# Optimization experiments

Hardware: AMD Instinct MI355X
Metric: run time of the kernel (lower is better)

Reference implementation:

```python
import jax, jax.numpy as jnp
import numpy as np

FIELD_DIMS = [26000] * 39
EMBED_DIM = 64
MLP_DIMS = [400, 400, 400]
BATCH = 16384
OFFSETS = jnp.asarray(np.concatenate(([0], np.cumsum(FIELD_DIMS)[:-1])), dtype=jnp.int32)
BN_INV = 1.0 / np.sqrt(1.0 + 1e-5)  # eval-mode BatchNorm1d: running_mean=0, running_var=1


def setup_inputs() -> dict:
    key = jax.random.key(0)
    ks = jax.random.split(key, 16)
    B, F, E = BATCH, len(FIELD_DIMS), EMBED_DIM
    V = sum(FIELD_DIMS)
    s = lambda k, shp, sc=0.05: (jax.random.normal(k, shp, jnp.float32) * sc)
    inp = {
        "x": jax.random.randint(ks[0], (B, F), 0, FIELD_DIMS[0], dtype=jnp.int32),
        "emb_table": s(ks[1], (V, E)),
        "lin_table": s(ks[2], (V, 1)),
        "lin_bias": jnp.zeros((1,), jnp.float32),
        "sparse_var": s(ks[3], (F, E), 0.1),
        "Wt": s(ks[4], (F, E, E)),  # per-field Linear weights, (out,in) layout
        "bt": jnp.zeros((F, E), jnp.float32),
    }
    dims = [F * E] + MLP_DIMS
    for i in range(3):
        inp[f"W{i+1}"] = s(ks[5 + i], (dims[i], dims[i + 1]))
        inp[f"b{i+1}"] = jnp.zeros((dims[i + 1],), jnp.float32)
        inp[f"g{i+1}"] = jnp.ones((dims[i + 1],), jnp.float32)
        inp[f"be{i+1}"] = jnp.zeros((dims[i + 1],), jnp.float32)
    inp["Wout"] = s(ks[9], (MLP_DIMS[-1], 1))
    inp["bout"] = jnp.zeros((1,), jnp.float32)
    return inp


def reference(x, emb_table, lin_table, lin_bias, sparse_var, Wt, bt,
              W1, b1, g1, be1, W2, b2, g2, be2, W3, b3, g3, be3, Wout, bout):
    B = x.shape[0]
    idx = x + OFFSETS[None, :]                       # (B, F) global vocab ids
    # sparse gate (detached in torch), eval-mode hard threshold mask
    sv = jax.nn.sigmoid(jax.lax.stop_gradient(sparse_var) * 15.0)
    sv = jnp.where(sv > 0.001, sv, 0.0)              # (F, E)
    embed_x = emb_table[idx] * sv                    # (B, F, E) gather + gate
    # per-field small Linear, batched as one einsum (torch: y = e @ W.T + b)
    trans = jnp.einsum('bfi,foi->bfo', embed_x, Wt) + bt  # (B, F, E)
    # FM second-order term
    sum_f = trans.sum(axis=1)                        # (B, E)
    fm = 0.5 * jnp.sum(sum_f * sum_f - (trans * trans).sum(axis=1),
                       axis=-1, keepdims=True)       # (B, 1)
    # first-order linear term
    lin = lin_table[idx].sum(axis=1) + lin_bias      # (B, 1)
    # MLP on flattened gated embeddings (Linear -> BN(eval) -> ReLU)
    h = embed_x.reshape(B, -1)
    for W, b, g, be in ((W1, b1, g1, be1), (W2, b2, g2, be2), (W3, b3, g3, be3)):
        h = jax.nn.relu((h @ W + b) * (BN_INV * g) + be)
    mlp = h @ Wout + bout                            # (B, 1)
    return jax.nn.sigmoid(jnp.squeeze(lin + fm + mlp, axis=1))  # (B,)
```

## Files before the change

kernel.cpp:

```cpp
#include <hip/hip_runtime.h>

#define BT 16384
#define NF 39
#define FD 26000

typedef unsigned short u16;
typedef unsigned int u32;
typedef short bf16x8 __attribute__((ext_vector_type(8)));
typedef float f32x4 __attribute__((ext_vector_type(4)));

__device__ __forceinline__ float bf2f(u16 h) {
  union { u32 u; float f; } v; v.u = ((u32)h) << 16; return v.f;
}
__device__ __forceinline__ u16 f2bf(float f) {
  union { float f; u32 u; } v; v.f = f;
  u32 r = v.u + 0x7fffu + ((v.u >> 16) & 1u);
  return (u16)(r >> 16);
}
__device__ __forceinline__ void gld16(const u16* g, u16* l) {
  __builtin_amdgcn_global_load_lds(
      (const __attribute__((address_space(1))) void*)g,
      (__attribute__((address_space(3))) void*)l, 16, 0, 0);
}

__global__ __launch_bounds__(256) void k_prep(
    const float* __restrict__ W1, u16* __restrict__ W1T,
    const float* __restrict__ W2, u16* __restrict__ W2T,
    const float* __restrict__ W3, u16* __restrict__ W3T,
    const float* __restrict__ Wt, u16* __restrict__ Wtb)
{
  int z = blockIdx.z;
  if (z == 3) {
    int idx = (blockIdx.y * 14 + blockIdx.x) * 256 + threadIdx.x;
    if (idx < NF * 4096) Wtb[idx] = f2bf(Wt[idx]);
    return;
  }
  const float* in = (z == 0) ? W1 : (z == 1) ? W2 : W3;
  u16* outp = (z == 0) ? W1T : (z == 1) ? W2T : W3T;
  int K = (z == 0) ? 2496 : 400;
  int Kpad = (z == 0) ? 2496 : 448;
  int r0 = blockIdx.y * 32, c0 = blockIdx.x * 32;
  if (r0 >= Kpad) return;
  __shared__ u16 t[32][33];
  int tx = threadIdx.x & 31, ty = threadIdx.x >> 5;
  for (int i = ty; i < 32; i += 8) {
    int r = r0 + i, c = c0 + tx;
    t[i][tx] = (r < K && c < 400) ? f2bf(in[(long)r * 400 + c]) : (u16)0;
  }
  __syncthreads();
  int r = r0 + tx;
  if (r < Kpad)
    for (int i = ty; i < 32; i += 8)
      outp[(long)(c0 + i) * Kpad + r] = t[tx][i];
}

__global__ __launch_bounds__(256) void k_embed(
    const int* __restrict__ x, const float* __restrict__ emb,
    const float* __restrict__ lin_table, const float* __restrict__ lin_bias,
    const float* __restrict__ sparse_var, const u16* __restrict__ Wtb,
    const float* __restrict__ bt, u16* __restrict__ h0, float* __restrict__ base)
{
  __shared__ u16                s_x[32 * NF];
  __shared__ float              s_sv[NF * 64];
  __shared__ float              s_bt[NF * 64];
  __shared__ __align__(16) u16  s_emb[2][32 * 72];
  __shared__ __align__(16) u16  s_wt[2][64 * 64];
  __shared__ float              s_fm[64];
  __shared__ float              s_lin[32];

  const int tid = threadIdx.x;
  const int b0 = blockIdx.x * 32;

  for (int i = tid; i < 32 * NF; i += 256) s_x[i] = (u16)x[b0 * NF + i];
  for (int i = tid; i < NF * 64; i += 256) {
    float v = sparse_var[i];
    float s = 1.0f / (1.0f + __expf(-15.0f * v));
    s_sv[i] = (s > 0.001f) ? s : 0.0f;
    s_bt[i] = bt[i];
  }
  __syncthreads();

  const int wave = tid >> 6, lane = tid & 63;
  const int quad = lane >> 4, c16 = lane & 15;
  const int mt = wave & 1, nh = wave >> 1;
  const int g_row = tid >> 3, g_c8 = (tid & 7) * 8;
  const int wrow = lane >> 3;
  const int wchk = (lane & 7) ^ wrow;

  float q[4] = {0.f, 0.f, 0.f, 0.f};
  float accS[2][4] = {{0.f,0.f,0.f,0.f},{0.f,0.f,0.f,0.f}};

  #pragma unroll
  for (int i = 0; i < 2; ++i) {
    int ii = wave * 2 + i;
    gld16(Wtb + (ii * 8 + wrow) * 64 + wchk * 8, &s_wt[0][ii * 512]);
  }
  {
    long gi = (long)((int)s_x[g_row * NF + 0]);
    float4 e0 = *(const float4*)&emb[gi * 64 + g_c8];
    float4 e1 = *(const float4*)&emb[gi * 64 + g_c8 + 4];
    union { uint4 v; u16 h[8]; } p;
    p.h[0] = f2bf(e0.x * s_sv[g_c8 + 0]);
    p.h[1] = f2bf(e0.y * s_sv[g_c8 + 1]);
    p.h[2] = f2bf(e0.z * s_sv[g_c8 + 2]);
    p.h[3] = f2bf(e0.w * s_sv[g_c8 + 3]);
    p.h[4] = f2bf(e1.x * s_sv[g_c8 + 4]);
    p.h[5] = f2bf(e1.y * s_sv[g_c8 + 5]);
    p.h[6] = f2bf(e1.z * s_sv[g_c8 + 6]);
    p.h[7] = f2bf(e1.w * s_sv[g_c8 + 7]);
    *(uint4*)&s_emb[0][g_row * 72 + g_c8] = p.v;
    *(uint4*)&h0[(long)(b0 + g_row) * 2496 + g_c8] = p.v;
  }
  __syncthreads();

  for (int f = 0; f < NF; ++f) {
    const int cur = f & 1, nxt = cur ^ 1;
    float4 e0, e1;
    const bool more = (f + 1) < NF;
    if (more) {
      #pragma unroll
      for (int i = 0; i < 2; ++i) {
        int ii = wave * 2 + i;
        gld16(Wtb + (f + 1) * 4096 + (ii * 8 + wrow) * 64 + wchk * 8,
              &s_wt[nxt][ii * 512]);
      }
      long gi = (long)((int)s_x[g_row * NF + f + 1] + (f + 1) * FD);
      e0 = *(const float4*)&emb[gi * 64 + g_c8];
      e1 = *(const float4*)&emb[gi * 64 + g_c8 + 4];
    }

    bf16x8 a0 = *(const bf16x8*)&s_emb[cur][(mt * 16 + c16) * 72 + quad * 8];
    bf16x8 a1 = *(const bf16x8*)&s_emb[cur][(mt * 16 + c16) * 72 + 32 + quad * 8];
    #pragma unroll
    for (int j = 0; j < 2; ++j) {
      int row = (nh * 2 + j) * 16 + c16;
      int pc0 = quad ^ (row & 7);
      int pc1 = (quad + 4) ^ (row & 7);
      bf16x8 bb0 = *(const bf16x8*)&s_wt[cur][row * 64 + pc0 * 8];
      bf16x8 bb1 = *(const bf16x8*)&s_wt[cur][row * 64 + pc1 * 8];
      f32x4 acc = {0.f, 0.f, 0.f, 0.f};
      acc = __builtin_amdgcn_mfma_f32_16x16x32_bf16(a0, bb0, acc, 0, 0, 0);
      acc = __builtin_amdgcn_mfma_f32_16x16x32_bf16(a1, bb1, acc, 0, 0, 0);
      float btv = s_bt[f * 64 + row];
      #pragma unroll
      for (int r = 0; r < 4; ++r) {
        float t = acc[r] + btv;
        accS[j][r] += t;
        q[r] += t * t;
      }
    }

    if (more) {
      union { uint4 v; u16 h[8]; } p;
      const float* sv = &s_sv[(f + 1) * 64 + g_c8];
      p.h[0] = f2bf(e0.x * sv[0]);
      p.h[1] = f2bf(e0.y * sv[1]);
      p.h[2] = f2bf(e0.z * sv[2]);
      p.h[3] = f2bf(e0.w * sv[3]);
      p.h[4] = f2bf(e1.x * sv[4]);
      p.h[5] = f2bf(e1.y * sv[5]);
      p.h[6] = f2bf(e1.z * sv[6]);
      p.h[7] = f2bf(e1.w * sv[7]);
      *(uint4*)&s_emb[nxt][g_row * 72 + g_c8] = p.v;
      *(uint4*)&h0[(long)(b0 + g_row) * 2496 + (f + 1) * 64 + g_c8] = p.v;
    }
    __syncthreads();
  }

  #pragma unroll
  for (int r = 0; r < 4; ++r) {
    float v = accS[0][r] * accS[0][r] + accS[1][r] * accS[1][r] - q[r];
    v += __shfl_xor(v, 1, 64);
    v += __shfl_xor(v, 2, 64);
    v += __shfl_xor(v, 4, 64);
    v += __shfl_xor(v, 8, 64);
    if (c16 == 0) s_fm[nh * 32 + mt * 16 + quad * 4 + r] = v;
  }
  {
    int row = tid >> 3, fi = tid & 7;
    float lv = 0.f;
    for (int f = fi; f < NF; f += 8)
      lv += lin_table[(int)s_x[row * NF + f] + f * FD];
    lv += __shfl_xor(lv, 1, 64);
    lv += __shfl_xor(lv, 2, 64);
    lv += __shfl_xor(lv, 4, 64);
    if (fi == 0) s_lin[row] = lv;
  }
  __syncthreads();
  if (tid < 32)
    base[b0 + tid] = s_lin[tid] + lin_bias[0]
                   + 0.5f * (s_fm[tid] + s_fm[32 + tid]);
}

__global__ __launch_bounds__(256) void k_gemm(
    const u16* __restrict__ A, int lda, const u16* __restrict__ Bt, int ldb,
    int kit, const float* __restrict__ bias, const float* __restrict__ g,
    const float* __restrict__ be, u16* __restrict__ C, int ldc)
{
  __shared__ __align__(16) u16 sA[128 * 64];
  __shared__ __align__(16) u16 sB[80 * 64];

  const int tid = threadIdx.x;
  int bid = blockIdx.x;
  int xcd = bid & 7;
  int j = bid >> 3;
  const int m0 = (xcd * 16 + j / 5) * 128;
  const int n0 = (j % 5) * 80;

  const int wave = tid >> 6, lane = tid & 63;
  const int quad = lane >> 4, c16 = lane & 15;

  const int srow = lane >> 3;
  const int sclog = (lane & 7) ^ (srow & 7);
  const u16* gA = A + (long)m0 * lda + sclog * 8;
  const u16* gB = Bt + (long)n0 * ldb + sclog * 8;

  f32x4 acc[2][5];
  #pragma unroll
  for (int mtt = 0; mtt < 2; ++mtt)
    #pragma unroll
    for (int nt = 0; nt < 5; ++nt) acc[mtt][nt] = {0.f, 0.f, 0.f, 0.f};

  for (int kk = 0; kk < kit; ++kk) {
    const int k0 = kk * 64;
    #pragma unroll
    for (int it = 0; it < 4; ++it) {
      int s = wave * 4 + it;
      gld16(gA + (long)(s * 8 + srow) * lda + k0, &sA[s * 512]);
    }
    gld16(gB + (long)(wave * 8 + srow) * ldb + k0, &sB[wave * 512]);
    gld16(gB + (long)((wave + 4) * 8 + srow) * ldb + k0, &sB[(wave + 4) * 512]);
    if (wave < 2)
      gld16(gB + (long)((wave + 8) * 8 + srow) * ldb + k0, &sB[(wave + 8) * 512]);
    __syncthreads();

    #pragma unroll
    for (int ks = 0; ks < 2; ++ks) {
      const int co = ((ks * 4 + quad) ^ (c16 & 7)) * 8;
      bf16x8 a0 = *(const bf16x8*)&sA[(wave * 32 + c16) * 64 + co];
      bf16x8 a1 = *(const bf16x8*)&sA[(wave * 32 + 16 + c16) * 64 + co];
      #pragma unroll
      for (int nt = 0; nt < 5; ++nt) {
        bf16x8 b = *(const bf16x8*)&sB[(nt * 16 + c16) * 64 + co];
        acc[0][nt] = __builtin_amdgcn_mfma_f32_16x16x32_bf16(a0, b, acc[0][nt], 0, 0, 0);
        acc[1][nt] = __builtin_amdgcn_mfma_f32_16x16x32_bf16(a1, b, acc[1][nt], 0, 0, 0);
      }
    }
    __syncthreads();
  }

  const float BN_INV = 0.9999950000374997f;
  #pragma unroll
  for (int nt = 0; nt < 5; ++nt) {
    int col = n0 + nt * 16 + c16;
    float bb = bias[col];
    float sc = BN_INV * g[col];
    float bv = be[col];
    #pragma unroll
    for (int mtt = 0; mtt < 2; ++mtt) {
      #pragma unroll
      for (int r = 0; r < 4; ++r) {
        int row = m0 + wave * 32 + mtt * 16 + quad * 4 + r;
        float y = (acc[mtt][nt][r] + bb) * sc + bv;
        y = fmaxf(y, 0.f);
        C[(long)row * ldc + col] = f2bf(y);
      }
    }
  }
  if (ldc > 400 && n0 == 320) {
    int npad = ldc - 400;
    for (int s = tid; s < 128 * npad; s += 256) {
      int rr = s / npad, cc = s % npad;
      C[(long)(m0 + rr) * ldc + 400 + cc] = 0;
    }
  }
}

__global__ __launch_bounds__(256) void k_final(
    const u16* __restrict__ h3, const float* __restrict__ Wout,
    const float* __restrict__ bout, const float* __restrict__ base,
    float* __restrict__ out)
{
  int wave = threadIdx.x >> 6, lane = threadIdx.x & 63;
  int b = blockIdx.x * 4 + wave;
  float s = 0.f;
  for (int jj = lane; jj < 400; jj += 64)
    s += bf2f(h3[(long)b * 448 + jj]) * Wout[jj];
  #pragma unroll
  for (int m = 32; m >= 1; m >>= 1) s += __shfl_xor(s, m, 64);
  if (lane == 0) {
    float z = s + base[b] + bout[0];
    out[b] = 1.0f / (1.0f + __expf(-z));
  }
}

extern "C" void kernel_launch(void* const* d_in, const int* in_sizes, int n_in,
                              void* d_out, int out_size, void* d_ws, size_t ws_size,
                              hipStream_t stream)
{
  const int*   x         = (const int*)d_in[0];
  const float* emb       = (const float*)d_in[1];
  const float* lin_table = (const float*)d_in[2];
  const float* lin_bias  = (const float*)d_in[3];
  const float* svar      = (const float*)d_in[4];
  const float* Wt        = (const float*)d_in[5];
  const float* bt        = (const float*)d_in[6];
  const float* W1  = (const float*)d_in[7];
  const float* b1  = (const float*)d_in[8];
  const float* g1  = (const float*)d_in[9];
  const float* be1 = (const float*)d_in[10];
  const float* W2  = (const float*)d_in[11];
  const float* b2  = (const float*)d_in[12];
  const float* g2  = (const float*)d_in[13];
  const float* be2 = (const float*)d_in[14];
  const float* W3  = (const float*)d_in[15];
  const float* b3  = (const float*)d_in[16];
  const float* g3  = (const float*)d_in[17];
  const float* be3 = (const float*)d_in[18];
  const float* Wo  = (const float*)d_in[19];
  const float* bo  = (const float*)d_in[20];

  char* ws = (char*)d_ws;
  size_t off = 0;
  u16* h0 = (u16*)(ws + off);     off += (size_t)BT * 2496 * 2;
  u16* h1 = (u16*)(ws + off);     off += (size_t)BT * 448 * 2;
  u16* h2 = (u16*)(ws + off);     off += (size_t)BT * 448 * 2;
  u16* h3 = (u16*)(ws + off);     off += (size_t)BT * 448 * 2;
  float* base = (float*)(ws + off); off += (size_t)BT * 4;
  u16* W1T = (u16*)(ws + off);    off += (size_t)448 * 2496 * 2;
  u16* W2T = (u16*)(ws + off);    off += (size_t)448 * 448 * 2;
  u16* W3T = (u16*)(ws + off);    off += (size_t)448 * 448 * 2;
  u16* Wtb = (u16*)(ws + off);    off += (size_t)NF * 4096 * 2;
  (void)ws_size; (void)in_sizes; (void)n_in; (void)out_size;

  k_prep<<<dim3(14, 78, 4), 256, 0, stream>>>(W1, W1T, W2, W2T, W3, W3T, Wt, Wtb);
  k_embed<<<512, 256, 0, stream>>>(x, emb, lin_table, lin_bias, svar, Wtb, bt,
                                   h0, base);
  k_gemm<<<640, 256, 0, stream>>>(h0, 2496, W1T, 2496, 39, b1, g1, be1, h1, 448);
  k_gemm<<<640, 256, 0, stream>>>(h1, 448, W2T, 448, 7, b2, g2, be2, h2, 448);
  k_gemm<<<640, 256, 0, stream>>>(h2, 448, W3T, 448, 7, b3, g3, be3, h3, 448);
  k_final<<<4096, 256, 0, stream>>>(h3, Wo, bo, base, (float*)d_out);
}
```

Before: 477.2 us.

## Fuse embedding gather, FM transform and first MLP layer into one kernel

The embedding/FM kernel now also computes the first MLP layer. For each field it streams the matching 64-wide K-slice of W1T into LDS with double buffering and accumulates a 64x448 output tile in registers, then applies bias, BN and ReLU and writes h1 directly. This removes the write and re-read of the large h0 activation buffer and one kernel launch. In exchange each block streams the whole W1T (256 blocks, 64 rows each, one block per CU by launch bounds), register pressure rises to 112 accumulators, and per-field Wt fragments are now read from global memory instead of LDS.

New measurement: 1.030 ms. +115.8%, slower.

```diff
diff --git a/kernel.cpp b/kernel.cpp
--- a/kernel.cpp
+++ b/kernel.cpp
@@ -54,142 +54,233 @@
       outp[(long)(c0 + i) * Kpad + r] = t[tx][i];
 }
 
-__global__ __launch_bounds__(256) void k_embed(
+__global__ __launch_bounds__(256, 1) void k_embed_mlp1(
     const int* __restrict__ x, const float* __restrict__ emb,
     const float* __restrict__ lin_table, const float* __restrict__ lin_bias,
     const float* __restrict__ sparse_var, const u16* __restrict__ Wtb,
-    const float* __restrict__ bt, u16* __restrict__ h0, float* __restrict__ base)
+    const float* __restrict__ bt, const u16* __restrict__ W1T,
+    const float* __restrict__ b1, const float* __restrict__ g1,
+    const float* __restrict__ be1, u16* __restrict__ h1,
+    float* __restrict__ base)
 {
-  __shared__ u16                s_x[32 * NF];
+  __shared__ u16                s_x[64 * NF];
   __shared__ float              s_sv[NF * 64];
-  __shared__ float              s_bt[NF * 64];
-  __shared__ __align__(16) u16  s_emb[2][32 * 72];
-  __shared__ __align__(16) u16  s_wt[2][64 * 64];
-  __shared__ float              s_fm[64];
-  __shared__ float              s_lin[32];
+  __shared__ __align__(16) u16  s_emb[2][64 * 72];
+  __shared__ __align__(16) u16  s_w1[2][448 * 64];
+  __shared__ float              s_fm[128];
+  __shared__ float              s_lin[64];
 
   const int tid = threadIdx.x;
-  const int b0 = blockIdx.x * 32;
-
-  for (int i = tid; i < 32 * NF; i += 256) s_x[i] = (u16)x[b0 * NF + i];
+  const int b0 = blockIdx.x * 64;
+
+  for (int i = tid; i < 64 * NF; i += 256) s_x[i] = (u16)x[b0 * NF + i];
   for (int i = tid; i < NF * 64; i += 256) {
     float v = sparse_var[i];
     float s = 1.0f / (1.0f + __expf(-15.0f * v));
     s_sv[i] = (s > 0.001f) ? s : 0.0f;
-    s_bt[i] = bt[i];
   }
   __syncthreads();
 
   const int wave = tid >> 6, lane = tid & 63;
   const int quad = lane >> 4, c16 = lane & 15;
-  const int mt = wave & 1, nh = wave >> 1;
-  const int g_row = tid >> 3, g_c8 = (tid & 7) * 8;
-  const int wrow = lane >> 3;
-  const int wchk = (lane & 7) ^ wrow;
-
-  float q[4] = {0.f, 0.f, 0.f, 0.f};
-  float accS[2][4] = {{0.f,0.f,0.f,0.f},{0.f,0.f,0.f,0.f}};
-
-  #pragma unroll
-  for (int i = 0; i < 2; ++i) {
-    int ii = wave * 2 + i;
-    gld16(Wtb + (ii * 8 + wrow) * 64 + wchk * 8, &s_wt[0][ii * 512]);
+  const int mh = wave >> 1, jh = wave & 1;
+  const int g_row = tid >> 2, g_c16 = (tid & 3) * 16;
+  const int srow = lane >> 3;
+  const u16* gW = W1T + ((lane & 7) ^ srow) * 8;
+
+  f32x4 acc[7][4];
+  #pragma unroll
+  for (int nt = 0; nt < 7; ++nt)
+    #pragma unroll
+    for (int m = 0; m < 4; ++m) acc[nt][m] = {0.f, 0.f, 0.f, 0.f};
+  float accS[2][2][4];
+  float q[2][4];
+  #pragma unroll
+  for (int ml = 0; ml < 2; ++ml)
+    #pragma unroll
+    for (int r = 0; r < 4; ++r) {
+      accS[ml][0][r] = 0.f; accS[ml][1][r] = 0.f; q[ml][r] = 0.f;
+    }
+
+  #pragma unroll
+  for (int it = 0; it < 14; ++it) {
+    int s = wave * 14 + it;
+    gld16(gW + (long)(s * 8 + srow) * 2496, &s_w1[0][s * 512]);
   }
   {
     long gi = (long)((int)s_x[g_row * NF + 0]);
-    float4 e0 = *(const float4*)&emb[gi * 64 + g_c8];
-    float4 e1 = *(const float4*)&emb[gi * 64 + g_c8 + 4];
-    union { uint4 v; u16 h[8]; } p;
-    p.h[0] = f2bf(e0.x * s_sv[g_c8 + 0]);
-    p.h[1] = f2bf(e0.y * s_sv[g_c8 + 1]);
-    p.h[2] = f2bf(e0.z * s_sv[g_c8 + 2]);
-    p.h[3] = f2bf(e0.w * s_sv[g_c8 + 3]);
-    p.h[4] = f2bf(e1.x * s_sv[g_c8 + 4]);
-    p.h[5] = f2bf(e1.y * s_sv[g_c8 + 5]);
-    p.h[6] = f2bf(e1.z * s_sv[g_c8 + 6]);
-    p.h[7] = f2bf(e1.w * s_sv[g_c8 + 7]);
-    *(uint4*)&s_emb[0][g_row * 72 + g_c8] = p.v;
-    *(uint4*)&h0[(long)(b0 + g_row) * 2496 + g_c8] = p.v;
+    const float* src = emb + gi * 64 + g_c16;
+    float4 e0 = *(const float4*)(src);
+    float4 e1 = *(const float4*)(src + 4);
+    float4 e2 = *(const float4*)(src + 8);
+    float4 e3 = *(const float4*)(src + 12);
+    const float* svp = &s_sv[g_c16];
+    float4 s0 = *(const float4*)(svp);
+    float4 s1 = *(const float4*)(svp + 4);
+    float4 s2 = *(const float4*)(svp + 8);
+    float4 s3 = *(const float4*)(svp + 12);
+    union { uint4 v; u16 h[8]; } p0, p1;
+    p0.h[0] = f2bf(e0.x * s0.x); p0.h[1] = f2bf(e0.y * s0.y);
+    p0.h[2] = f2bf(e0.z * s0.z); p0.h[3] = f2bf(e0.w * s0.w);
+    p0.h[4] = f2bf(e1.x * s1.x); p0.h[5] = f2bf(e1.y * s1.y);
+    p0.h[6] = f2bf(e1.z * s1.z); p0.h[7] = f2bf(e1.w * s1.w);
+    p1.h[0] = f2bf(e2.x * s2.x); p1.h[1] = f2bf(e2.y * s2.y);
+    p1.h[2] = f2bf(e2.z * s2.z); p1.h[3] = f2bf(e2.w * s2.w);
+    p1.h[4] = f2bf(e3.x * s3.x); p1.h[5] = f2bf(e3.y * s3.y);
+    p1.h[6] = f2bf(e3.z * s3.z); p1.h[7] = f2bf(e3.w * s3.w);
+    *(uint4*)&s_emb[0][g_row * 72 + g_c16] = p0.v;
+    *(uint4*)&s_emb[0][g_row * 72 + g_c16 + 8] = p1.v;
   }
   __syncthreads();
 
   for (int f = 0; f < NF; ++f) {
     const int cur = f & 1, nxt = cur ^ 1;
-    float4 e0, e1;
     const bool more = (f + 1) < NF;
+
     if (more) {
       #pragma unroll
-      for (int i = 0; i < 2; ++i) {
-        int ii = wave * 2 + i;
-        gld16(Wtb + (f + 1) * 4096 + (ii * 8 + wrow) * 64 + wchk * 8,
-              &s_wt[nxt][ii * 512]);
-      }
+      for (int it = 0; it < 14; ++it) {
+        int s = wave * 14 + it;
+        gld16(gW + (long)(s * 8 + srow) * 2496 + (f + 1) * 64,
+              &s_w1[nxt][s * 512]);
+      }
+    }
+
+    bf16x8 bwt[2][2];
+    float btv[2];
+    #pragma unroll
+    for (int j = 0; j < 2; ++j) {
+      int o = (jh * 2 + j) * 16 + c16;
+      bwt[j][0] = *(const bf16x8*)(Wtb + f * 4096 + o * 64 + quad * 8);
+      bwt[j][1] = *(const bf16x8*)(Wtb + f * 4096 + o * 64 + 32 + quad * 8);
+      btv[j] = bt[f * 64 + o];
+    }
+
+    float4 e0, e1, e2, e3;
+    if (more) {
       long gi = (long)((int)s_x[g_row * NF + f + 1] + (f + 1) * FD);
-      e0 = *(const float4*)&emb[gi * 64 + g_c8];
-      e1 = *(const float4*)&emb[gi * 64 + g_c8 + 4];
-    }
-
-    bf16x8 a0 = *(const bf16x8*)&s_emb[cur][(mt * 16 + c16) * 72 + quad * 8];
-    bf16x8 a1 = *(const bf16x8*)&s_emb[cur][(mt * 16 + c16) * 72 + 32 + quad * 8];
-    #pragma unroll
-    for (int j = 0; j < 2; ++j) {
-      int row = (nh * 2 + j) * 16 + c16;
-      int pc0 = quad ^ (row & 7);
-      int pc1 = (quad + 4) ^ (row & 7);
-      bf16x8 bb0 = *(const bf16x8*)&s_wt[cur][row * 64 + pc0 * 8];
-      bf16x8 bb1 = *(const bf16x8*)&s_wt[cur][row * 64 + pc1 * 8];
-      f32x4 acc = {0.f, 0.f, 0.f, 0.f};
-      acc = __builtin_amdgcn_mfma_f32_16x16x32_bf16(a0, bb0, acc, 0, 0, 0);
-      acc = __builtin_amdgcn_mfma_f32_16x16x32_bf16(a1, bb1, acc, 0, 0, 0);
-      float btv = s_bt[f * 64 + row];
-      #pragma unroll
-      for (int r = 0; r < 4; ++r) {
-        float t = acc[r] + btv;
-        accS[j][r] += t;
-        q[r] += t * t;
+      const float* src = emb + gi * 64 + g_c16;
+      e0 = *(const float4*)(src);
+      e1 = *(const float4*)(src + 4);
+      e2 = *(const float4*)(src + 8);
+      e3 = *(const float4*)(src + 12);
+    }
+
+    bf16x8 a[4][2];
+    #pragma unroll
+    for (int m = 0; m < 4; ++m) {
+      #pragma unroll
+      for (int ks = 0; ks < 2; ++ks)
+        a[m][ks] = *(const bf16x8*)
+            &s_emb[cur][(m * 16 + c16) * 72 + ks * 32 + quad * 8];
+    }
+
+    #pragma unroll
+    for (int nt = 0; nt < 7; ++nt) {
+      int n = wave * 112 + nt * 16 + c16;
+      #pragma unroll
+      for (int ks = 0; ks < 2; ++ks) {
+        bf16x8 b = *(const bf16x8*)
+            &s_w1[cur][n * 64 + (((ks * 4 + quad) ^ (c16 & 7)) * 8)];
+        #pragma unroll
+        for (int m = 0; m < 4; ++m)
+          acc[nt][m] = __builtin_amdgcn_mfma_f32_16x16x32_bf16(
+              a[m][ks], b, acc[nt][m], 0, 0, 0);
+      }
+    }
+
+    #pragma unroll
+    for (int mloc = 0; mloc < 2; ++mloc) {
+      int m = mh * 2 + mloc;
+      #pragma unroll
+      for (int j = 0; j < 2; ++j) {
+        f32x4 t = {0.f, 0.f, 0.f, 0.f};
+        t = __builtin_amdgcn_mfma_f32_16x16x32_bf16(a[m][0], bwt[j][0], t, 0, 0, 0);
+        t = __builtin_amdgcn_mfma_f32_16x16x32_bf16(a[m][1], bwt[j][1], t, 0, 0, 0);
+        #pragma unroll
+        for (int r = 0; r < 4; ++r) {
+          float tv = t[r] + btv[j];
+          accS[mloc][j][r] += tv;
+          q[mloc][r] += tv * tv;
+        }
       }
     }
 
     if (more) {
-      union { uint4 v; u16 h[8]; } p;
-      const float* sv = &s_sv[(f + 1) * 64 + g_c8];
-      p.h[0] = f2bf(e0.x * sv[0]);
-      p.h[1] = f2bf(e0.y * sv[1]);
-      p.h[2] = f2bf(e0.z * sv[2]);
-      p.h[3] = f2bf(e0.w * sv[3]);
-      p.h[4] = f2bf(e1.x * sv[4]);
-      p.h[5] = f2bf(e1.y * sv[5]);
-      p.h[6] = f2bf(e1.z * sv[6]);
-      p.h[7] = f2bf(e1.w * sv[7]);
-      *(uint4*)&s_emb[nxt][g_row * 72 + g_c8] = p.v;
-      *(uint4*)&h0[(long)(b0 + g_row) * 2496 + (f + 1) * 64 + g_c8] = p.v;
+      const float* svp = &s_sv[(f + 1) * 64 + g_c16];
+      float4 s0 = *(const float4*)(svp);
+      float4 s1 = *(const float4*)(svp + 4);
+      float4 s2 = *(const float4*)(svp + 8);
+      float4 s3 = *(const float4*)(svp + 12);
+      union { uint4 v; u16 h[8]; } p0, p1;
+      p0.h[0] = f2bf(e0.x * s0.x); p0.h[1] = f2bf(e0.y * s0.y);
+      p0.h[2] = f2bf(e0.z * s0.z); p0.h[3] = f2bf(e0.w * s0.w);
+      p0.h[4] = f2bf(e1.x * s1.x); p0.h[5] = f2bf(e1.y * s1.y);
+      p0.h[6] = f2bf(e1.z * s1.z); p0.h[7] = f2bf(e1.w * s1.w);
+      p1.h[0] = f2bf(e2.x * s2.x); p1.h[1] = f2bf(e2.y * s2.y);
+      p1.h[2] = f2bf(e2.z * s2.z); p1.h[3] = f2bf(e2.w * s2.w);
+      p1.h[4] = f2bf(e3.x * s3.x); p1.h[5] = f2bf(e3.y * s3.y);
+      p1.h[6] = f2bf(e3.z * s3.z); p1.h[7] = f2bf(e3.w * s3.w);
+      *(uint4*)&s_emb[nxt][g_row * 72 + g_c16] = p0.v;
+      *(uint4*)&s_emb[nxt][g_row * 72 + g_c16 + 8] = p1.v;
     }
     __syncthreads();
   }
 
-  #pragma unroll
-  for (int r = 0; r < 4; ++r) {
-    float v = accS[0][r] * accS[0][r] + accS[1][r] * accS[1][r] - q[r];
-    v += __shfl_xor(v, 1, 64);
-    v += __shfl_xor(v, 2, 64);
-    v += __shfl_xor(v, 4, 64);
-    v += __shfl_xor(v, 8, 64);
-    if (c16 == 0) s_fm[nh * 32 + mt * 16 + quad * 4 + r] = v;
+  const float BN_INV = 0.9999950000374997f;
+  #pragma unroll
+  for (int nt = 0; nt < 7; ++nt) {
+    int col = wave * 112 + nt * 16 + c16;
+    if (col < 400) {
+      float bb = b1[col];
+      float sc = BN_INV * g1[col];
+      float bv = be1[col];
+      #pragma unroll
+      for (int m = 0; m < 4; ++m) {
+        #pragma unroll
+        for (int r = 0; r < 4; ++r) {
+          int row = b0 + m * 16 + quad * 4 + r;
+          float y = (acc[nt][m][r] + bb) * sc + bv;
+          y = fmaxf(y, 0.f);
+          h1[(long)row * 448 + col] = f2bf(y);
+        }
+      }
+    } else {
+      #pragma unroll
+      for (int m = 0; m < 4; ++m)
+        #pragma unroll
+        for (int r = 0; r < 4; ++r)
+          h1[(long)(b0 + m * 16 + quad * 4 + r) * 448 + col] = 0;
+    }
+  }
+
+  #pragma unroll
+  for (int mloc = 0; mloc < 2; ++mloc) {
+    #pragma unroll
+    for (int r = 0; r < 4; ++r) {
+      float v = accS[mloc][0][r] * accS[mloc][0][r]
+              + accS[mloc][1][r] * accS[mloc][1][r] - q[mloc][r];
+      v += __shfl_xor(v, 1, 64);
+      v += __shfl_xor(v, 2, 64);
+      v += __shfl_xor(v, 4, 64);
+      v += __shfl_xor(v, 8, 64);
+      if (c16 == 0)
+        s_fm[jh * 64 + (mh * 2 + mloc) * 16 + quad * 4 + r] = v;
+    }
   }
   {
-    int row = tid >> 3, fi = tid & 7;
+    int row = tid >> 2, fi = tid & 3;
     float lv = 0.f;
-    for (int f = fi; f < NF; f += 8)
+    for (int f = fi; f < NF; f += 4)
       lv += lin_table[(int)s_x[row * NF + f] + f * FD];
     lv += __shfl_xor(lv, 1, 64);
     lv += __shfl_xor(lv, 2, 64);
-    lv += __shfl_xor(lv, 4, 64);
     if (fi == 0) s_lin[row] = lv;
   }
   __syncthreads();
-  if (tid < 32)
+  if (tid < 64)
     base[b0 + tid] = s_lin[tid] + lin_bias[0]
-                   + 0.5f * (s_fm[tid] + s_fm[32 + tid]);
+                   + 0.5f * (s_fm[tid] + s_fm[64 + tid]);
 }
 
 __global__ __launch_bounds__(256) void k_gemm(
@@ -322,7 +413,6 @@
 
   char* ws = (char*)d_ws;
   size_t off = 0;
-  u16* h0 = (u16*)(ws + off);     off += (size_t)BT * 2496 * 2;
   u16* h1 = (u16*)(ws + off);     off += (size_t)BT * 448 * 2;
   u16* h2 = (u16*)(ws + off);     off += (size_t)BT * 448 * 2;
   u16* h3 = (u16*)(ws + off);     off += (size_t)BT * 448 * 2;
@@ -334,9 +424,8 @@
   (void)ws_size; (void)in_sizes; (void)n_in; (void)out_size;
 
   k_prep<<<dim3(14, 78, 4), 256, 0, stream>>>(W1, W1T, W2, W2T, W3, W3T, Wt, Wtb);
-  k_embed<<<512, 256, 0, stream>>>(x, emb, lin_table, lin_bias, svar, Wtb, bt,
-                                   h0, base);
-  k_gemm<<<640, 256, 0, stream>>>(h0, 2496, W1T, 2496, 39, b1, g1, be1, h1, 448);
+  k_embed_mlp1<<<256, 256, 0, stream>>>(x, emb, lin_table, lin_bias, svar, Wtb,
+                                        bt, W1T, b1, g1, be1, h1, base);
   k_gemm<<<640, 256, 0, stream>>>(h1, 448, W2T, 448, 7, b2, g2, be2, h2, 448);
   k_gemm<<<640, 256, 0, stream>>>(h2, 448, W3T, 448, 7, b3, g3, be3, h3, 448);
   k_final<<<4096, 256, 0, stream>>>(h3, Wo, bo, base, (float*)d_out);
```

## Fuse embedding gather with first MLP GEMM to skip materializing h0

Applied to the files above, without the earlier changes.

The embedding kernel now multiplies each field's gated 32x64 embedding tile directly against the matching W1T slice. Both the per-field transform weights and the W1 fragments are read straight from global memory into registers, and results accumulate into 32x448 tiles held in registers. The BN and ReLU epilogue is applied before writing h1, so the separate first GEMM launch and the large bf16 h0 write and re-read are removed. In exchange each 32-row block streams all of W1T through L2 with a small M tile and no LDS staging. That means much more L2 traffic, higher register pressure and exposed load latency inside the per-field loop.

Measured after the change: 533.9 us. 1.12x slower.

```diff
diff --git a/kernel.cpp b/kernel.cpp
--- a/kernel.cpp
+++ b/kernel.cpp
@@ -54,18 +54,20 @@
       outp[(long)(c0 + i) * Kpad + r] = t[tx][i];
 }
 
-__global__ __launch_bounds__(256) void k_embed(
+__global__ __launch_bounds__(256) void k_embed_mlp1(
     const int* __restrict__ x, const float* __restrict__ emb,
     const float* __restrict__ lin_table, const float* __restrict__ lin_bias,
     const float* __restrict__ sparse_var, const u16* __restrict__ Wtb,
-    const float* __restrict__ bt, u16* __restrict__ h0, float* __restrict__ base)
+    const float* __restrict__ bt, const u16* __restrict__ W1T,
+    const float* __restrict__ b1, const float* __restrict__ g1,
+    const float* __restrict__ be1, u16* __restrict__ h1,
+    float* __restrict__ base)
 {
   __shared__ u16                s_x[32 * NF];
   __shared__ float              s_sv[NF * 64];
   __shared__ float              s_bt[NF * 64];
   __shared__ __align__(16) u16  s_emb[2][32 * 72];
-  __shared__ __align__(16) u16  s_wt[2][64 * 64];
-  __shared__ float              s_fm[64];
+  __shared__ float              s_fm[4][32];
   __shared__ float              s_lin[32];
 
   const int tid = threadIdx.x;
@@ -82,19 +84,23 @@
 
   const int wave = tid >> 6, lane = tid & 63;
   const int quad = lane >> 4, c16 = lane & 15;
-  const int mt = wave & 1, nh = wave >> 1;
   const int g_row = tid >> 3, g_c8 = (tid & 7) * 8;
-  const int wrow = lane >> 3;
-  const int wchk = (lane & 7) ^ wrow;
-
-  float q[4] = {0.f, 0.f, 0.f, 0.f};
-  float accS[2][4] = {{0.f,0.f,0.f,0.f},{0.f,0.f,0.f,0.f}};
-
-  #pragma unroll
-  for (int i = 0; i < 2; ++i) {
-    int ii = wave * 2 + i;
-    gld16(Wtb + (ii * 8 + wrow) * 64 + wchk * 8, &s_wt[0][ii * 512]);
-  }
+
+  const u16* w1p = W1T + (long)(wave * 112 + c16) * 2496 + quad * 8;
+  const u16* wtp = Wtb + (long)(wave * 16 + c16) * 64 + quad * 8;
+
+  f32x4 acc[7][2];
+  #pragma unroll
+  for (int nt = 0; nt < 7; ++nt) {
+    acc[nt][0] = {0.f, 0.f, 0.f, 0.f};
+    acc[nt][1] = {0.f, 0.f, 0.f, 0.f};
+  }
+  float accS[2][4], q[2][4];
+  #pragma unroll
+  for (int m = 0; m < 2; ++m)
+    #pragma unroll
+    for (int r = 0; r < 4; ++r) { accS[m][r] = 0.f; q[m][r] = 0.f; }
+
   {
     long gi = (long)((int)s_x[g_row * NF + 0]);
     float4 e0 = *(const float4*)&emb[gi * 64 + g_c8];
@@ -109,50 +115,61 @@
     p.h[6] = f2bf(e1.z * s_sv[g_c8 + 6]);
     p.h[7] = f2bf(e1.w * s_sv[g_c8 + 7]);
     *(uint4*)&s_emb[0][g_row * 72 + g_c8] = p.v;
-    *(uint4*)&h0[(long)(b0 + g_row) * 2496 + g_c8] = p.v;
   }
   __syncthreads();
 
   for (int f = 0; f < NF; ++f) {
     const int cur = f & 1, nxt = cur ^ 1;
+    const bool more = (f + 1) < NF;
+
+    bf16x8 bwt0 = *(const bf16x8*)(wtp + f * 4096);
+    bf16x8 bwt1 = *(const bf16x8*)(wtp + f * 4096 + 32);
+    float btv = s_bt[f * 64 + wave * 16 + c16];
+
     float4 e0, e1;
-    const bool more = (f + 1) < NF;
     if (more) {
-      #pragma unroll
-      for (int i = 0; i < 2; ++i) {
-        int ii = wave * 2 + i;
-        gld16(Wtb + (f + 1) * 4096 + (ii * 8 + wrow) * 64 + wchk * 8,
-              &s_wt[nxt][ii * 512]);
-      }
       long gi = (long)((int)s_x[g_row * NF + f + 1] + (f + 1) * FD);
       e0 = *(const float4*)&emb[gi * 64 + g_c8];
       e1 = *(const float4*)&emb[gi * 64 + g_c8 + 4];
     }
 
-    bf16x8 a0 = *(const bf16x8*)&s_emb[cur][(mt * 16 + c16) * 72 + quad * 8];
-    bf16x8 a1 = *(const bf16x8*)&s_emb[cur][(mt * 16 + c16) * 72 + 32 + quad * 8];
-    #pragma unroll
-    for (int j = 0; j < 2; ++j) {
-      int row = (nh * 2 + j) * 16 + c16;
-      int pc0 = quad ^ (row & 7);
-      int pc1 = (quad + 4) ^ (row & 7);
-      bf16x8 bb0 = *(const bf16x8*)&s_wt[cur][row * 64 + pc0 * 8];
-      bf16x8 bb1 = *(const bf16x8*)&s_wt[cur][row * 64 + pc1 * 8];
-      f32x4 acc = {0.f, 0.f, 0.f, 0.f};
-      acc = __builtin_amdgcn_mfma_f32_16x16x32_bf16(a0, bb0, acc, 0, 0, 0);
-      acc = __builtin_amdgcn_mfma_f32_16x16x32_bf16(a1, bb1, acc, 0, 0, 0);
-      float btv = s_bt[f * 64 + row];
+    bf16x8 a[2][2];
+    #pragma unroll
+    for (int m = 0; m < 2; ++m)
+      #pragma unroll
+      for (int ks = 0; ks < 2; ++ks)
+        a[m][ks] = *(const bf16x8*)
+            &s_emb[cur][(m * 16 + c16) * 72 + ks * 32 + quad * 8];
+
+    const u16* w1f = w1p + f * 64;
+    #pragma unroll
+    for (int nt = 0; nt < 7; ++nt) {
+      #pragma unroll
+      for (int ks = 0; ks < 2; ++ks) {
+        bf16x8 b = *(const bf16x8*)(w1f + (long)nt * 16 * 2496 + ks * 32);
+        acc[nt][0] = __builtin_amdgcn_mfma_f32_16x16x32_bf16(
+            a[0][ks], b, acc[nt][0], 0, 0, 0);
+        acc[nt][1] = __builtin_amdgcn_mfma_f32_16x16x32_bf16(
+            a[1][ks], b, acc[nt][1], 0, 0, 0);
+      }
+    }
+
+    #pragma unroll
+    for (int m = 0; m < 2; ++m) {
+      f32x4 t = {0.f, 0.f, 0.f, 0.f};
+      t = __builtin_amdgcn_mfma_f32_16x16x32_bf16(a[m][0], bwt0, t, 0, 0, 0);
+      t = __builtin_amdgcn_mfma_f32_16x16x32_bf16(a[m][1], bwt1, t, 0, 0, 0);
       #pragma unroll
       for (int r = 0; r < 4; ++r) {
-        float t = acc[r] + btv;
-        accS[j][r] += t;
-        q[r] += t * t;
+        float tv = t[r] + btv;
+        accS[m][r] += tv;
+        q[m][r] += tv * tv;
       }
     }
 
     if (more) {
+      const float* sv = &s_sv[(f + 1) * 64 + g_c8];
       union { uint4 v; u16 h[8]; } p;
-      const float* sv = &s_sv[(f + 1) * 64 + g_c8];
       p.h[0] = f2bf(e0.x * sv[0]);
       p.h[1] = f2bf(e0.y * sv[1]);
       p.h[2] = f2bf(e0.z * sv[2]);
@@ -162,19 +179,48 @@
       p.h[6] = f2bf(e1.z * sv[6]);
       p.h[7] = f2bf(e1.w * sv[7]);
       *(uint4*)&s_emb[nxt][g_row * 72 + g_c8] = p.v;
-      *(uint4*)&h0[(long)(b0 + g_row) * 2496 + (f + 1) * 64 + g_c8] = p.v;
     }
     __syncthreads();
   }
 
-  #pragma unroll
-  for (int r = 0; r < 4; ++r) {
-    float v = accS[0][r] * accS[0][r] + accS[1][r] * accS[1][r] - q[r];
-    v += __shfl_xor(v, 1, 64);
-    v += __shfl_xor(v, 2, 64);
-    v += __shfl_xor(v, 4, 64);
-    v += __shfl_xor(v, 8, 64);
-    if (c16 == 0) s_fm[nh * 32 + mt * 16 + quad * 4 + r] = v;
+  const float BN_INV = 0.9999950000374997f;
+  #pragma unroll
+  for (int nt = 0; nt < 7; ++nt) {
+    int col = wave * 112 + nt * 16 + c16;
+    if (col < 400) {
+      float bb = b1[col];
+      float sc = BN_INV * g1[col];
+      float bv = be1[col];
+      #pragma unroll
+      for (int m = 0; m < 2; ++m) {
+        #pragma unroll
+        for (int r = 0; r < 4; ++r) {
+          int row = b0 + m * 16 + quad * 4 + r;
+          float y = (acc[nt][m][r] + bb) * sc + bv;
+          y = fmaxf(y, 0.f);
+          h1[(long)row * 448 + col] = f2bf(y);
+        }
+      }
+    } else {
+      #pragma unroll
+      for (int m = 0; m < 2; ++m)
+        #pragma unroll
+        for (int r = 0; r < 4; ++r)
+          h1[(long)(b0 + m * 16 + quad * 4 + r) * 448 + col] = 0;
+    }
+  }
+
+  #pragma unroll
+  for (int m = 0; m < 2; ++m) {
+    #pragma unroll
+    for (int r = 0; r < 4; ++r) {
+      float v = accS[m][r] * accS[m][r] - q[m][r];
+      v += __shfl_xor(v, 1, 64);
+      v += __shfl_xor(v, 2, 64);
+      v += __shfl_xor(v, 4, 64);
+      v += __shfl_xor(v, 8, 64);
+      if (c16 == 0) s_fm[wave][m * 16 + quad * 4 + r] = v;
+    }
   }
   {
     int row = tid >> 3, fi = tid & 7;
@@ -189,7 +235,8 @@
   __syncthreads();
   if (tid < 32)
     base[b0 + tid] = s_lin[tid] + lin_bias[0]
-                   + 0.5f * (s_fm[tid] + s_fm[32 + tid]);
+                   + 0.5f * (s_fm[0][tid] + s_fm[1][tid]
+                           + s_fm[2][tid] + s_fm[3][tid]);
 }
 
 __global__ __launch_bounds__(256) void k_gemm(
@@ -322,7 +369,6 @@
 
   char* ws = (char*)d_ws;
   size_t off = 0;
-  u16* h0 = (u16*)(ws + off);     off += (size_t)BT * 2496 * 2;
   u16* h1 = (u16*)(ws + off);     off += (size_t)BT * 448 * 2;
   u16* h2 = (u16*)(ws + off);     off += (size_t)BT * 448 * 2;
   u16* h3 = (u16*)(ws + off);     off += (size_t)BT * 448 * 2;
@@ -334,9 +380,8 @@
   (void)ws_size; (void)in_sizes; (void)n_in; (void)out_size;
 
   k_prep<<<dim3(14, 78, 4), 256, 0, stream>>>(W1, W1T, W2, W2T, W3, W3T, Wt, Wtb);
-  k_embed<<<512, 256, 0, stream>>>(x, emb, lin_table, lin_bias, svar, Wtb, bt,
-                                   h0, base);
-  k_gemm<<<640, 256, 0, stream>>>(h0, 2496, W1T, 2496, 39, b1, g1, be1, h1, 448);
+  k_embed_mlp1<<<512, 256, 0, stream>>>(x, emb, lin_table, lin_bias, svar, Wtb,
+                                        bt, W1T, b1, g1, be1, h1, base);
   k_gemm<<<640, 256, 0, stream>>>(h1, 448, W2T, 448, 7, b2, g2, be2, h2, 448);
   k_gemm<<<640, 256, 0, stream>>>(h2, 448, W3T, 448, 7, b3, g3, be3, h3, 448);
   k_final<<<4096, 256, 0, stream>>>(h3, Wo, bo, base, (float*)d_out);
```

## Split embed kernel fields across waves with register-resident operands and no per-field barriers

Applied to the files above, without the earlier changes.

The embedding/FM kernel now handles 16 rows per block, and each wave takes a strided subset of fields instead of all waves cooperating on every field. Embedding rows are gathered straight into registers as MFMA A-operands, with a one-step register prefetch. Per-field weights are read from global memory, so the LDS double buffering and the per-field __syncthreads are gone. Partial FM sums are reduced across waves through shared memory at the end. The intent is to remove 39 block barriers and raise parallelism (twice as many blocks, launch bounds set for occupancy), at the cost of more global weight traffic per block.

Result: slower. 503.9 us (+5.6%).

```diff
diff --git a/kernel.cpp b/kernel.cpp
--- a/kernel.cpp
+++ b/kernel.cpp
@@ -54,24 +54,24 @@
       outp[(long)(c0 + i) * Kpad + r] = t[tx][i];
 }
 
-__global__ __launch_bounds__(256) void k_embed(
+__global__ __launch_bounds__(256, 4) void k_embed(
     const int* __restrict__ x, const float* __restrict__ emb,
     const float* __restrict__ lin_table, const float* __restrict__ lin_bias,
     const float* __restrict__ sparse_var, const u16* __restrict__ Wtb,
     const float* __restrict__ bt, u16* __restrict__ h0, float* __restrict__ base)
 {
-  __shared__ u16                s_x[32 * NF];
-  __shared__ float              s_sv[NF * 64];
-  __shared__ float              s_bt[NF * 64];
-  __shared__ __align__(16) u16  s_emb[2][32 * 72];
-  __shared__ __align__(16) u16  s_wt[2][64 * 64];
-  __shared__ float              s_fm[64];
-  __shared__ float              s_lin[32];
+  __shared__ u16   s_x[16 * NF];
+  __shared__ float s_sv[NF * 64];
+  __shared__ float s_bt[NF * 64];
+  __shared__ float s_acc[3][16][64];
+  __shared__ float s_q[3][4][64];
+  __shared__ float s_fm[16];
+  __shared__ float s_lin[16];
 
   const int tid = threadIdx.x;
-  const int b0 = blockIdx.x * 32;
-
-  for (int i = tid; i < 32 * NF; i += 256) s_x[i] = (u16)x[b0 * NF + i];
+  const int b0 = blockIdx.x * 16;
+
+  for (int i = tid; i < 16 * NF; i += 256) s_x[i] = (u16)x[b0 * NF + i];
   for (int i = tid; i < NF * 64; i += 256) {
     float v = sparse_var[i];
     float s = 1.0f / (1.0f + __expf(-15.0f * v));
@@ -82,114 +82,117 @@
 
   const int wave = tid >> 6, lane = tid & 63;
   const int quad = lane >> 4, c16 = lane & 15;
-  const int mt = wave & 1, nh = wave >> 1;
-  const int g_row = tid >> 3, g_c8 = (tid & 7) * 8;
-  const int wrow = lane >> 3;
-  const int wchk = (lane & 7) ^ wrow;
-
-  float q[4] = {0.f, 0.f, 0.f, 0.f};
-  float accS[2][4] = {{0.f,0.f,0.f,0.f},{0.f,0.f,0.f,0.f}};
-
-  #pragma unroll
-  for (int i = 0; i < 2; ++i) {
-    int ii = wave * 2 + i;
-    gld16(Wtb + (ii * 8 + wrow) * 64 + wchk * 8, &s_wt[0][ii * 512]);
-  }
+
+  float accS[4][4], q[4];
+  #pragma unroll
+  for (int cg = 0; cg < 4; ++cg)
+    #pragma unroll
+    for (int r = 0; r < 4; ++r) accS[cg][r] = 0.f;
+  #pragma unroll
+  for (int r = 0; r < 4; ++r) q[r] = 0.f;
+
+  const u16* xrow = &s_x[c16 * NF];
+  u16* hrow = h0 + (long)(b0 + c16) * 2496 + quad * 8;
+
+  float4 c0, c1, c2, c3;
   {
-    long gi = (long)((int)s_x[g_row * NF + 0]);
-    float4 e0 = *(const float4*)&emb[gi * 64 + g_c8];
-    float4 e1 = *(const float4*)&emb[gi * 64 + g_c8 + 4];
-    union { uint4 v; u16 h[8]; } p;
-    p.h[0] = f2bf(e0.x * s_sv[g_c8 + 0]);
-    p.h[1] = f2bf(e0.y * s_sv[g_c8 + 1]);
-    p.h[2] = f2bf(e0.z * s_sv[g_c8 + 2]);
-    p.h[3] = f2bf(e0.w * s_sv[g_c8 + 3]);
-    p.h[4] = f2bf(e1.x * s_sv[g_c8 + 4]);
-    p.h[5] = f2bf(e1.y * s_sv[g_c8 + 5]);
-    p.h[6] = f2bf(e1.z * s_sv[g_c8 + 6]);
-    p.h[7] = f2bf(e1.w * s_sv[g_c8 + 7]);
-    *(uint4*)&s_emb[0][g_row * 72 + g_c8] = p.v;
-    *(uint4*)&h0[(long)(b0 + g_row) * 2496 + g_c8] = p.v;
-  }
-  __syncthreads();
-
-  for (int f = 0; f < NF; ++f) {
-    const int cur = f & 1, nxt = cur ^ 1;
-    float4 e0, e1;
-    const bool more = (f + 1) < NF;
-    if (more) {
-      #pragma unroll
-      for (int i = 0; i < 2; ++i) {
-        int ii = wave * 2 + i;
-        gld16(Wtb + (f + 1) * 4096 + (ii * 8 + wrow) * 64 + wchk * 8,
-              &s_wt[nxt][ii * 512]);
+    long gi = (long)((int)xrow[wave] + wave * FD);
+    const float* src = emb + gi * 64 + quad * 8;
+    c0 = *(const float4*)(src);
+    c1 = *(const float4*)(src + 4);
+    c2 = *(const float4*)(src + 32);
+    c3 = *(const float4*)(src + 36);
+  }
+
+  for (int f = wave; f < NF; f += 4) {
+    float4 n0, n1, n2, n3;
+    if (f + 4 < NF) {
+      long gi = (long)((int)xrow[f + 4] + (f + 4) * FD);
+      const float* src = emb + gi * 64 + quad * 8;
+      n0 = *(const float4*)(src);
+      n1 = *(const float4*)(src + 4);
+      n2 = *(const float4*)(src + 32);
+      n3 = *(const float4*)(src + 36);
+    }
+
+    const float* sv = &s_sv[f * 64 + quad * 8];
+    union { uint4 v; u16 h[8]; } pa, pb;
+    pa.h[0] = f2bf(c0.x * sv[0]);  pa.h[1] = f2bf(c0.y * sv[1]);
+    pa.h[2] = f2bf(c0.z * sv[2]);  pa.h[3] = f2bf(c0.w * sv[3]);
+    pa.h[4] = f2bf(c1.x * sv[4]);  pa.h[5] = f2bf(c1.y * sv[5]);
+    pa.h[6] = f2bf(c1.z * sv[6]);  pa.h[7] = f2bf(c1.w * sv[7]);
+    pb.h[0] = f2bf(c2.x * sv[32]); pb.h[1] = f2bf(c2.y * sv[33]);
+    pb.h[2] = f2bf(c2.z * sv[34]); pb.h[3] = f2bf(c2.w * sv[35]);
+    pb.h[4] = f2bf(c3.x * sv[36]); pb.h[5] = f2bf(c3.y * sv[37]);
+    pb.h[6] = f2bf(c3.z * sv[38]); pb.h[7] = f2bf(c3.w * sv[39]);
+    *(uint4*)(hrow + f * 64) = pa.v;
+    *(uint4*)(hrow + f * 64 + 32) = pb.v;
+    bf16x8 a0 = *(bf16x8*)&pa;
+    bf16x8 a1 = *(bf16x8*)&pb;
+
+    const u16* wf = Wtb + f * 4096 + c16 * 64 + quad * 8;
+    const float* btf = &s_bt[f * 64 + c16];
+    #pragma unroll
+    for (int cg = 0; cg < 4; ++cg) {
+      bf16x8 bb0 = *(const bf16x8*)(wf + cg * 1024);
+      bf16x8 bb1 = *(const bf16x8*)(wf + cg * 1024 + 32);
+      f32x4 t = {0.f, 0.f, 0.f, 0.f};
+      t = __builtin_amdgcn_mfma_f32_16x16x32_bf16(a0, bb0, t, 0, 0, 0);
+      t = __builtin_amdgcn_mfma_f32_16x16x32_bf16(a1, bb1, t, 0, 0, 0);
+      float btv = btf[cg * 16];
+      #pragma unroll
+      for (int r = 0; r < 4; ++r) {
+        float tv = t[r] + btv;
+        accS[cg][r] += tv;
+        q[r] += tv * tv;
       }
-      long gi = (long)((int)s_x[g_row * NF + f + 1] + (f + 1) * FD);
-      e0 = *(const float4*)&emb[gi * 64 + g_c8];
-      e1 = *(const float4*)&emb[gi * 64 + g_c8 + 4];
-    }
-
-    bf16x8 a0 = *(const bf16x8*)&s_emb[cur][(mt * 16 + c16) * 72 + quad * 8];
-    bf16x8 a1 = *(const bf16x8*)&s_emb[cur][(mt * 16 + c16) * 72 + 32 + quad * 8];
-    #pragma unroll
-    for (int j = 0; j < 2; ++j) {
-      int row = (nh * 2 + j) * 16 + c16;
-      int pc0 = quad ^ (row & 7);
-      int pc1 = (quad + 4) ^ (row & 7);
-      bf16x8 bb0 = *(const bf16x8*)&s_wt[cur][row * 64 + pc0 * 8];
-      bf16x8 bb1 = *(const bf16x8*)&s_wt[cur][row * 64 + pc1 * 8];
-      f32x4 acc = {0.f, 0.f, 0.f, 0.f};
-      acc = __builtin_amdgcn_mfma_f32_16x16x32_bf16(a0, bb0, acc, 0, 0, 0);
-      acc = __builtin_amdgcn_mfma_f32_16x16x32_bf16(a1, bb1, acc, 0, 0, 0);
-      float btv = s_bt[f * 64 + row];
-      #pragma unroll
-      for (int r = 0; r < 4; ++r) {
-        float t = acc[r] + btv;
-        accS[j][r] += t;
-        q[r] += t * t;
-      }
-    }
-
-    if (more) {
-      union { uint4 v; u16 h[8]; } p;
-      const float* sv = &s_sv[(f + 1) * 64 + g_c8];
-      p.h[0] = f2bf(e0.x * sv[0]);
-      p.h[1] = f2bf(e0.y * sv[1]);
-      p.h[2] = f2bf(e0.z * sv[2]);
-      p.h[3] = f2bf(e0.w * sv[3]);
-      p.h[4] = f2bf(e1.x * sv[4]);
-      p.h[5] = f2bf(e1.y * sv[5]);
-      p.h[6] = f2bf(e1.z * sv[6]);
-      p.h[7] = f2bf(e1.w * sv[7]);
-      *(uint4*)&s_emb[nxt][g_row * 72 + g_c8] = p.v;
-      *(uint4*)&h0[(long)(b0 + g_row) * 2496 + (f + 1) * 64 + g_c8] = p.v;
-    }
-    __syncthreads();
-  }
-
-  #pragma unroll
-  for (int r = 0; r < 4; ++r) {
-    float v = accS[0][r] * accS[0][r] + accS[1][r] * accS[1][r] - q[r];
-    v += __shfl_xor(v, 1, 64);
-    v += __shfl_xor(v, 2, 64);
-    v += __shfl_xor(v, 4, 64);
-    v += __shfl_xor(v, 8, 64);
-    if (c16 == 0) s_fm[nh * 32 + mt * 16 + quad * 4 + r] = v;
+    }
+    c0 = n0; c1 = n1; c2 = n2; c3 = n3;
+  }
+
+  if (wave != 0) {
+    #pragma unroll
+    for (int cg = 0; cg < 4; ++cg)
+      #pragma unroll
+      for (int r = 0; r < 4; ++r)
+        s_acc[wave - 1][cg * 4 + r][lane] = accS[cg][r];
+    #pragma unroll
+    for (int r = 0; r < 4; ++r) s_q[wave - 1][r][lane] = q[r];
   }
   {
-    int row = tid >> 3, fi = tid & 7;
+    int lrow = tid >> 4, fi = tid & 15;
     float lv = 0.f;
-    for (int f = fi; f < NF; f += 8)
-      lv += lin_table[(int)s_x[row * NF + f] + f * FD];
+    for (int f = fi; f < NF; f += 16)
+      lv += lin_table[(int)s_x[lrow * NF + f] + f * FD];
     lv += __shfl_xor(lv, 1, 64);
     lv += __shfl_xor(lv, 2, 64);
     lv += __shfl_xor(lv, 4, 64);
-    if (fi == 0) s_lin[row] = lv;
+    lv += __shfl_xor(lv, 8, 64);
+    if (fi == 0) s_lin[lrow] = lv;
   }
   __syncthreads();
-  if (tid < 32)
-    base[b0 + tid] = s_lin[tid] + lin_bias[0]
-                   + 0.5f * (s_fm[tid] + s_fm[32 + tid]);
+  if (wave == 0) {
+    #pragma unroll
+    for (int r = 0; r < 4; ++r) {
+      float qT = q[r] + s_q[0][r][lane] + s_q[1][r][lane] + s_q[2][r][lane];
+      float v = 0.f;
+      #pragma unroll
+      for (int cg = 0; cg < 4; ++cg) {
+        float aT = accS[cg][r] + s_acc[0][cg * 4 + r][lane]
+                 + s_acc[1][cg * 4 + r][lane] + s_acc[2][cg * 4 + r][lane];
+        v += aT * aT;
+      }
+      v -= qT;
+      v += __shfl_xor(v, 1, 64);
+      v += __shfl_xor(v, 2, 64);
+      v += __shfl_xor(v, 4, 64);
+      v += __shfl_xor(v, 8, 64);
+      if (c16 == 0) s_fm[quad * 4 + r] = v;
+    }
+  }
+  __syncthreads();
+  if (tid < 16)
+    base[b0 + tid] = s_lin[tid] + lin_bias[0] + 0.5f * s_fm[tid];
 }
 
 __global__ __launch_bounds__(256) void k_gemm(
@@ -334,8 +337,8 @@
   (void)ws_size; (void)in_sizes; (void)n_in; (void)out_size;
 
   k_prep<<<dim3(14, 78, 4), 256, 0, stream>>>(W1, W1T, W2, W2T, W3, W3T, Wt, Wtb);
-  k_embed<<<512, 256, 0, stream>>>(x, emb, lin_table, lin_bias, svar, Wtb, bt,
-                                   h0, base);
+  k_embed<<<1024, 256, 0, stream>>>(x, emb, lin_table, lin_bias, svar, Wtb, bt,
+                                    h0, base);
   k_gemm<<<640, 256, 0, stream>>>(h0, 2496, W1T, 2496, 39, b1, g1, be1, h1, 448);
   k_gemm<<<640, 256, 0, stream>>>(h1, 448, W2T, 448, 7, b2, g2, be2, h2, 448);
   k_gemm<<<640, 256, 0, stream>>>(h2, 448, W3T, 448, 7, b3, g3, be3, h3, 448);
```
